# Kernel optimization log

Hardware: AMD Instinct MI355X
Metric: run time of the kernel (lower is better)

Reference implementation:

```python
import jax, jax.numpy as jnp
import numpy as np
import math

B, S, HID = 2, 2048, 2048
NH, NKV, HD = 16, 4, 128
ROPE_BASE = 10000.0

def _rope(x, position_ids):
    # x: [B, H, S, HD], position_ids: [B, S]
    half = HD // 2
    inv_freq = 1.0 / (ROPE_BASE ** (jnp.arange(0, half, dtype=jnp.float32) / half))
    freqs = position_ids.astype(jnp.float32)[:, :, None] * inv_freq[None, None, :]  # [B,S,half]
    cos = jnp.cos(freqs)[:, None, :, :]  # [B,1,S,half]
    sin = jnp.sin(freqs)[:, None, :, :]
    x1, x2 = x[..., :half], x[..., half:]
    return jnp.concatenate([x1 * cos - x2 * sin, x2 * cos + x1 * sin], axis=-1)

def setup_inputs() -> dict:
    key = jax.random.key(0)
    k1, k2, k3 = jax.random.split(key, 3)
    x = jax.random.normal(k1, (B, S, HID), dtype=jnp.float32)
    position_ids = jnp.broadcast_to(jnp.arange(S, dtype=jnp.int64 if jax.config.jax_enable_x64 else jnp.int32)[None, :], (B, S))
    causal = jnp.tril(jnp.ones((S, S), dtype=bool))
    mask = jnp.where(causal, 0.0, -1e9).astype(jnp.float32)[None, None, :, :]
    w_qkv = jax.random.normal(k2, (NH * HD + 2 * NKV * HD, HID), dtype=jnp.float32) * 0.02
    w_o = jax.random.normal(k3, (HID, HID), dtype=jnp.float32) * 0.02
    return {"x": x, "position_ids": position_ids, "mask": mask, "w_qkv": w_qkv, "w_o": w_o}

def reference(x, position_ids, mask, w_qkv, w_o):
    qkv = x @ w_qkv.T  # [B,S,3072]
    q_dim, kv_dim = NH * HD, NKV * HD
    q = qkv[..., :q_dim].reshape(B, S, NH, HD).transpose(0, 2, 1, 3)          # [B,NH,S,HD]
    k = qkv[..., q_dim:q_dim + kv_dim].reshape(B, S, NKV, HD).transpose(0, 2, 1, 3)
    v = qkv[..., q_dim + kv_dim:].reshape(B, S, NKV, HD).transpose(0, 2, 1, 3)
    q = _rope(q, position_ids)
    k = _rope(k, position_ids)
    n_rep = NH // NKV
    k = jnp.repeat(k, n_rep, axis=1)  # [B,NH,S,HD]
    v = jnp.repeat(v, n_rep, axis=1)
    scores = jnp.einsum('bhqd,bhkd->bhqk', q, k) / math.sqrt(HD) + mask
    attn = jax.nn.softmax(scores, axis=-1)  # dropout p=0.0 -> identity
    out = jnp.einsum('bhqk,bhkd->bhqd', attn, v)
    out = out.transpose(0, 2, 1, 3).reshape(B, S, HID)
    return out @ w_o.T
```

## Files before the change

kernel.cpp:

```cpp
#include <hip/hip_runtime.h>
#include <hip/hip_bf16.h>
#include <cstdint>
#include <cstddef>

typedef unsigned short u16;
typedef __attribute__((ext_vector_type(8))) __bf16 bf16x8;
typedef __attribute__((ext_vector_type(4))) float floatx4;

#define B_    2
#define S_    2048
#define HID_  2048
#define NH_   16
#define NKV_  4
#define HD_   128
#define QKVN_ 3072

__device__ __forceinline__ float bf2f(u16 u) {
  union { unsigned int i; float f; } v; v.i = ((unsigned int)u) << 16; return v.f;
}
__device__ __forceinline__ u16 f2bf(float f) {
  union { float f; unsigned int i; } v; v.f = f;
  unsigned int u = v.i;
  return (u16)((u + 0x7fffu + ((u >> 16) & 1u)) >> 16);
}

#define GLOAD_LDS16(gp, lp)                                                  \
  __builtin_amdgcn_global_load_lds(                                          \
      (__attribute__((address_space(1))) void*)(gp),                         \
      (__attribute__((address_space(3))) void*)(lp), 16, 0, 0)

__global__ __launch_bounds__(256)
void cast_f32_bf16(const float* __restrict__ in, u16* __restrict__ out, int n)
{
  const int i = (blockIdx.x * 256 + threadIdx.x) * 8;
  if (i >= n) return;
  const float4 a = *(const float4*)(in + i);
  const float4 b = *(const float4*)(in + i + 4);
  union { u16 h[8]; uint4 v; } o;
  o.h[0] = f2bf(a.x); o.h[1] = f2bf(a.y); o.h[2] = f2bf(a.z); o.h[3] = f2bf(a.w);
  o.h[4] = f2bf(b.x); o.h[5] = f2bf(b.y); o.h[6] = f2bf(b.z); o.h[7] = f2bf(b.w);
  *(uint4*)(out + i) = o.v;
}

template <bool F32OUT>
__global__ __launch_bounds__(256, 3)
void gemm_bt_128(const u16* __restrict__ A, const u16* __restrict__ W,
                 void* __restrict__ Cv, int N, int K, int lda, int ldc)
{
  __shared__ __align__(16) u16 lA[128 * 64];
  __shared__ __align__(16) u16 lB[128 * 64];
  const int tid  = threadIdx.x;
  const int w    = tid >> 6, ln = tid & 63;
  const int quad = ln >> 4,  l15 = ln & 15;
  const int m0 = blockIdx.y * 128, n0 = blockIdx.x * 128;
  const int waveM = (w >> 1) * 64, waveN = (w & 1) * 64;

  const floatx4 vzero = {0.f, 0.f, 0.f, 0.f};
  floatx4 acc[4][4];
#pragma unroll
  for (int i = 0; i < 4; ++i)
#pragma unroll
    for (int j = 0; j < 4; ++j) acc[i][j] = vzero;

  for (int k0 = 0; k0 < K; k0 += 64) {
    __syncthreads();
#pragma unroll
    for (int p = 0; p < 4; ++p) {
      const int L = (p * 4 + w) * 64 + ln;
      const int row = L >> 3, c = L & 7;
      GLOAD_LDS16(A + (size_t)(m0 + row) * lda + k0 + c * 8, lA + L * 8);
      GLOAD_LDS16(W + (size_t)(n0 + row) * K   + k0 + c * 8, lB + L * 8);
    }
    __syncthreads();
#pragma unroll
    for (int kk = 0; kk < 64; kk += 32) {
      bf16x8 aF[4], bF[4];
      const int cbase = (kk >> 3) + quad;
#pragma unroll
      for (int t = 0; t < 4; ++t) {
        const int rowA = waveM + t * 16 + l15;
        aF[t] = *(const bf16x8*)(lA + rowA * 64 + cbase * 8);
        const int rowB = waveN + t * 16 + l15;
        bF[t] = *(const bf16x8*)(lB + rowB * 64 + cbase * 8);
      }
#pragma unroll
      for (int i = 0; i < 4; ++i)
#pragma unroll
        for (int j = 0; j < 4; ++j)
          acc[i][j] = __builtin_amdgcn_mfma_f32_16x16x32_bf16(aF[i], bF[j], acc[i][j], 0, 0, 0);
    }
  }
#pragma unroll
  for (int i = 0; i < 4; ++i)
#pragma unroll
    for (int r = 0; r < 4; ++r) {
      const int row = m0 + waveM + i * 16 + quad * 4 + r;
      if (F32OUT) {
        float* cp = (float*)Cv + (size_t)row * ldc + n0 + waveN + l15;
#pragma unroll
        for (int j = 0; j < 4; ++j) cp[j * 16] = acc[i][j][r];
      } else {
        u16* cp = (u16*)Cv + (size_t)row * ldc + n0 + waveN + l15;
#pragma unroll
        for (int j = 0; j < 4; ++j) cp[j * 16] = f2bf(acc[i][j][r]);
      }
    }
}

__global__ __launch_bounds__(256)
void rope_inplace(u16* __restrict__ qkv)
{
  const int s = blockIdx.x, b = blockIdx.y;
  const int tid = threadIdx.x;
  __shared__ float cs[64], sn[64];
  if (tid < 64) {
    const float inv = powf(10000.0f, -((float)tid) / 64.0f);
    float s_, c_;
    sincosf((float)s * inv, &s_, &c_);
    cs[tid] = c_; sn[tid] = s_;
  }
  __syncthreads();
  u16* base = qkv + ((size_t)b * S_ + s) * QKVN_;
  for (int p = tid; p < NH_ * 64; p += 256) {
    const int h = p >> 6, i = p & 63;
    u16* hp = base + h * 128;
    const float x1 = bf2f(hp[i]);
    const float x2 = bf2f(hp[64 + i]);
    hp[i]      = f2bf(x1 * cs[i] - x2 * sn[i]);
    hp[64 + i] = f2bf(x2 * cs[i] + x1 * sn[i]);
  }
  for (int p = tid; p < NKV_ * 64; p += 256) {
    const int h = p >> 6, i = p & 63;
    u16* hp = base + NH_ * HD_ + h * 128;
    const float x1 = bf2f(hp[i]);
    const float x2 = bf2f(hp[64 + i]);
    hp[i]      = f2bf(x1 * cs[i] - x2 * sn[i]);
    hp[64 + i] = f2bf(x2 * cs[i] + x1 * sn[i]);
  }
}

__global__ __launch_bounds__(256)
void v_transpose(const u16* __restrict__ qkv, u16* __restrict__ vt)
{
  const int s0  = blockIdx.x * 64;
  const int kvh = blockIdx.y;
  const int b   = blockIdx.z;
  const int tid = threadIdx.x;
  __shared__ u16 lT[128 * 73];

  const u16* vsrc = qkv + ((size_t)b * S_ + s0) * QKVN_
                    + NH_ * HD_ + NKV_ * HD_ + kvh * HD_;
#pragma unroll
  for (int p = 0; p < 4; ++p) {
    const int idx = p * 256 + tid;
    const int r = idx >> 4, c = idx & 15;
    union { uint4 v; u16 h[8]; } u;
    u.v = *(const uint4*)(vsrc + (size_t)r * QKVN_ + c * 8);
#pragma unroll
    for (int j = 0; j < 8; ++j)
      lT[(c * 8 + j) * 73 + r] = u.h[j];
  }
  __syncthreads();
  u16* vdst = vt + ((size_t)(b * NKV_ + kvh) * HD_) * S_ + s0;
#pragma unroll
  for (int p = 0; p < 4; ++p) {
    const int idx = p * 256 + tid;
    const int d = idx >> 3, rc = idx & 7;
    union { uint4 v; u16 h[8]; } o;
#pragma unroll
    for (int j = 0; j < 8; ++j)
      o.h[j] = lT[d * 73 + rc * 8 + j];
    *(uint4*)(vdst + (size_t)d * S_ + rc * 8) = o.v;
  }
}

#define LPP 68
#define KSLOT(key, s) ((key) * 128 + (((s) ^ ((key) & 7)) * 8))
#define VSLOT(d, s)   ((d) * 64  + (((s) ^ ((d) & 7)) * 8))

__global__ __launch_bounds__(256, 2)
void flash_attn(u16* __restrict__ qkv, const u16* __restrict__ vt_ws)
{
  const int pi = blockIdx.x;
  const int h  = blockIdx.y;
  const int b  = blockIdx.z;
  const int tid  = threadIdx.x;
  const int w    = tid >> 6, ln = tid & 63;
  const int quad = ln >> 4,  l15 = ln & 15;
  const int kvh  = h >> 2;

  const int qtA = 31 - pi, qtB = pi;
  const int itA = qtA + 1;
  const int nIt = itA + qtB + 1;

  __shared__ __align__(16) u16 lK[2][64 * 128];
  __shared__ __align__(16) u16 lVt[2][128 * 64];
  __shared__ __align__(16) u16 lP[4][16 * LPP];

  const float scale = 0.08838834764831845f;
  const u16* kbase = qkv + (size_t)b * S_ * QKVN_ + NH_ * HD_ + kvh * HD_;
  const u16* vbase = vt_ws + (size_t)(b * NKV_ + kvh) * HD_ * S_;
  const floatx4 vzero = {0.f, 0.f, 0.f, 0.f};

  bf16x8 qFA[4], qFB[4];
  {
    const u16* qpA = qkv + ((size_t)(b * S_) + qtA * 64 + w * 16 + l15) * QKVN_ + h * HD_;
    const u16* qpB = qkv + ((size_t)(b * S_) + qtB * 64 + w * 16 + l15) * QKVN_ + h * HD_;
#pragma unroll
    for (int c = 0; c < 4; ++c) {
      qFA[c] = *(const bf16x8*)(qpA + c * 32 + quad * 8);
      qFB[c] = *(const bf16x8*)(qpB + c * 32 + quad * 8);
    }
  }

  float m_i[4], l_i[4];
  floatx4 Oacc[8];
#pragma unroll
  for (int r = 0; r < 4; ++r) { m_i[r] = -1e30f; l_i[r] = 0.f; }
#pragma unroll
  for (int t = 0; t < 8; ++t) Oacc[t] = vzero;

  bf16x8 qF[4];
#pragma unroll
  for (int c = 0; c < 4; ++c) qF[c] = qFA[c];
  int qtC = qtA;
  int qrow0 = qtA * 64 + w * 16;

#pragma unroll
  for (int p = 0; p < 4; ++p) {
    const int idx = (w * 4 + p) * 64 + ln;
    const int key = idx >> 4, ks = idx & 15;
    GLOAD_LDS16(kbase + (size_t)key * QKVN_ + ((ks ^ (key & 7)) * 8),
                lK[0] + (w * 4 + p) * 512);
    const int d = idx >> 3, vs = idx & 7;
    GLOAD_LDS16(vbase + (size_t)d * S_ + ((vs ^ (d & 7)) * 8),
                lVt[0] + (w * 4 + p) * 512);
  }

#pragma unroll 1
  for (int it = 0; it < nIt; ++it) {
    const int ktC = (it < itA) ? it : (it - itA);
    const u16* lKc = lK[it & 1];
    const u16* lVc = lVt[it & 1];
    const bool pf = (it + 1 < nIt);
    if (pf) {
      const int ktN = (it + 1 < itA) ? (it + 1) : (it + 1 - itA);
      u16* lKn = lK[(it + 1) & 1];
      u16* lVn = lVt[(it + 1) & 1];
#pragma unroll
      for (int p = 0; p < 4; ++p) {
        const int idx = (w * 4 + p) * 64 + ln;
        const int key = idx >> 4, ks = idx & 15;
        GLOAD_LDS16(kbase + (size_t)(ktN * 64 + key) * QKVN_ + ((ks ^ (key & 7)) * 8),
                    lKn + (w * 4 + p) * 512);
        const int d = idx >> 3, vs = idx & 7;
        GLOAD_LDS16(vbase + (size_t)d * S_ + ktN * 64 + ((vs ^ (d & 7)) * 8),
                    lVn + (w * 4 + p) * 512);
      }
      asm volatile("s_waitcnt vmcnt(8)" ::: "memory");
    } else {
      asm volatile("s_waitcnt vmcnt(0)" ::: "memory");
    }
    __builtin_amdgcn_s_barrier();
    __builtin_amdgcn_sched_barrier(0);

    floatx4 sc[4];
    __builtin_amdgcn_s_setprio(1);
#pragma unroll
    for (int nt = 0; nt < 4; ++nt) {
      floatx4 a = vzero;
      const int keyloc = nt * 16 + l15;
#pragma unroll
      for (int c = 0; c < 4; ++c) {
        const bf16x8 kF = *(const bf16x8*)(lKc + KSLOT(keyloc, c * 4 + quad));
        a = __builtin_amdgcn_mfma_f32_16x16x32_bf16(qF[c], kF, a, 0, 0, 0);
      }
      sc[nt] = a;
    }
    __builtin_amdgcn_s_setprio(0);

    float pr[4][4];
#pragma unroll
    for (int r = 0; r < 4; ++r) {
      const int qrow = qrow0 + quad * 4 + r;
      float s[4];
#pragma unroll
      for (int nt = 0; nt < 4; ++nt) {
        const int key0 = ktC * 64 + nt * 16 + l15;
        s[nt] = sc[nt][r] * scale + ((key0 <= qrow) ? 0.f : -1e9f);
      }
      float mx = fmaxf(fmaxf(s[0], s[1]), fmaxf(s[2], s[3]));
#pragma unroll
      for (int off = 1; off < 16; off <<= 1) mx = fmaxf(mx, __shfl_xor(mx, off, 64));
      const float mn = fmaxf(m_i[r], mx);
      const float alpha = __expf(m_i[r] - mn);
      float sm = 0.f;
#pragma unroll
      for (int nt = 0; nt < 4; ++nt) {
        const float p = __expf(s[nt] - mn);
        pr[nt][r] = p;
        sm += p;
      }
#pragma unroll
      for (int off = 1; off < 16; off <<= 1) sm += __shfl_xor(sm, off, 64);
      l_i[r] = l_i[r] * alpha + sm;
      m_i[r] = mn;
#pragma unroll
      for (int t = 0; t < 8; ++t) Oacc[t][r] *= alpha;
    }

#pragma unroll
    for (int nt = 0; nt < 4; ++nt)
#pragma unroll
      for (int r = 0; r < 4; ++r)
        lP[w][(quad * 4 + r) * LPP + nt * 16 + l15] = f2bf(pr[nt][r]);

    {
      const bf16x8 pF0 = *(const bf16x8*)(&lP[w][l15 * LPP + quad * 8]);
      const bf16x8 pF1 = *(const bf16x8*)(&lP[w][l15 * LPP + 32 + quad * 8]);
      __builtin_amdgcn_s_setprio(1);
#pragma unroll
      for (int t = 0; t < 8; ++t) {
        const int d = t * 16 + l15;
        const bf16x8 vF0 = *(const bf16x8*)(lVc + VSLOT(d, quad));
        const bf16x8 vF1 = *(const bf16x8*)(lVc + VSLOT(d, 4 + quad));
        Oacc[t] = __builtin_amdgcn_mfma_f32_16x16x32_bf16(pF0, vF0, Oacc[t], 0, 0, 0);
        Oacc[t] = __builtin_amdgcn_mfma_f32_16x16x32_bf16(pF1, vF1, Oacc[t], 0, 0, 0);
      }
      __builtin_amdgcn_s_setprio(0);
    }

    if (ktC == qtC) {
      float linv[4];
#pragma unroll
      for (int r = 0; r < 4; ++r) linv[r] = 1.0f / l_i[r];
#pragma unroll
      for (int t = 0; t < 8; ++t) {
        const int d = t * 16 + l15;
#pragma unroll
        for (int r = 0; r < 4; ++r) {
          const int qrow = qrow0 + quad * 4 + r;
          qkv[((size_t)(b * S_ + qrow)) * QKVN_ + h * HD_ + d] =
              f2bf(Oacc[t][r] * linv[r]);
        }
      }
      if (pf) {
        qtC = qtB;
        qrow0 = qtB * 64 + w * 16;
#pragma unroll
        for (int c = 0; c < 4; ++c) qF[c] = qFB[c];
#pragma unroll
        for (int r = 0; r < 4; ++r) { m_i[r] = -1e30f; l_i[r] = 0.f; }
#pragma unroll
        for (int t = 0; t < 8; ++t) Oacc[t] = vzero;
      }
    }

    __builtin_amdgcn_s_barrier();
  }
}

extern "C" void kernel_launch(void* const* d_in, const int* in_sizes, int n_in,
                              void* d_out, int out_size, void* d_ws, size_t ws_size,
                              hipStream_t stream)
{
  (void)in_sizes; (void)n_in; (void)out_size; (void)ws_size;
  const float* x     = (const float*)d_in[0];
  const float* w_qkv = (const float*)d_in[3];
  const float* w_o   = (const float*)d_in[4];
  float* out = (float*)d_out;

  const int nX  = B_ * S_ * HID_;
  const int nWq = QKVN_ * HID_;
  const int nWo = HID_ * HID_;

  u16* ws    = (u16*)d_ws;
  u16* qkv   = ws;
  u16* slotW = qkv + (size_t)(B_ * S_) * QKVN_;
  u16* xb    = (u16*)d_out;
  u16* vt_ws = (u16*)d_out;

  const dim3 blk(256);
  cast_f32_bf16<<<nX  / 2048, blk, 0, stream>>>(x,     xb,    nX);
  cast_f32_bf16<<<nWq / 2048, blk, 0, stream>>>(w_qkv, slotW, nWq);
  gemm_bt_128<false><<<dim3(QKVN_ / 128, (B_ * S_) / 128), blk, 0, stream>>>(
      xb, slotW, qkv, QKVN_, HID_, HID_, QKVN_);
  rope_inplace<<<dim3(S_, B_), blk, 0, stream>>>(qkv);
  v_transpose<<<dim3(S_ / 64, NKV_, B_), blk, 0, stream>>>(qkv, vt_ws);
  cast_f32_bf16<<<nWo / 2048, blk, 0, stream>>>(w_o, slotW, nWo);
  flash_attn<<<dim3(16, NH_, B_), blk, 0, stream>>>(qkv, vt_ws);
  gemm_bt_128<true><<<dim3(HID_ / 128, (B_ * S_) / 128), blk, 0, stream>>>(
      qkv, slotW, out, HID_, HID_, QKVN_, HID_);
}
```

Before: 341.2 us.

## Add 256x256-tile 512-thread GEMM for QKV projection with double-buffered LDS

Adds a new GEMM kernel with 256x256 output tiles, 8 waves, and double-buffered global-to-LDS loads in 128KB of dynamic shared memory, and uses it for the QKV projection. Larger tiles raise arithmetic intensity and cut global traffic per FLOP. The grid shrinks to 12x16=192 blocks, which may underfill a 256-CU device, and 128KB of LDS per block limits occupancy. The old 128-tile kernel's launch bounds also change from 3 to 2 blocks per CU.

Result: no change. 340.2 us (-0.3%).

```diff
diff --git a/kernel.cpp b/kernel.cpp
--- a/kernel.cpp
+++ b/kernel.cpp
@@ -43,7 +43,115 @@
 }
 
 template <bool F32OUT>
-__global__ __launch_bounds__(256, 3)
+__global__ __launch_bounds__(512, 2)
+void gemm_bt_256(const u16* __restrict__ A, const u16* __restrict__ W,
+                 void* __restrict__ Cv, int K, int lda, int ldc)
+{
+  extern __shared__ __align__(16) u16 smem[];
+  u16* lA = smem;
+  u16* lB = smem + 32768;
+
+  const int tid  = threadIdx.x;
+  const int wid  = tid >> 6, ln = tid & 63;
+  const int quad = ln >> 4,  l15 = ln & 15;
+  const int wr = wid >> 2, wc = wid & 3;
+  const int m0 = blockIdx.y * 256, n0 = blockIdx.x * 256;
+
+  const floatx4 vzero = {0.f, 0.f, 0.f, 0.f};
+  floatx4 acc[8][4];
+#pragma unroll
+  for (int i = 0; i < 8; ++i)
+#pragma unroll
+    for (int j = 0; j < 4; ++j) acc[i][j] = vzero;
+
+  const int NT = K >> 6;
+
+#define STAGE256(kt, buf)                                                     \
+  {                                                                           \
+    _Pragma("unroll")                                                         \
+    for (int p = 0; p < 4; ++p) {                                             \
+      const int L = (wid * 4 + p) * 64 + ln;                                  \
+      const int row = L >> 3, c = L & 7;                                      \
+      const int cs = (c ^ (row & 7)) * 8;                                     \
+      GLOAD_LDS16(A + (size_t)(m0 + row) * lda + (kt) * 64 + cs,              \
+                  lA + (buf) * 16384 + L * 8);                                \
+      GLOAD_LDS16(W + (size_t)(n0 + row) * K + (kt) * 64 + cs,                \
+                  lB + (buf) * 16384 + L * 8);                                \
+    }                                                                         \
+  }
+
+  STAGE256(0, 0);
+
+#pragma unroll 1
+  for (int t = 0; t < NT; ++t) {
+    if (t + 1 < NT) {
+      STAGE256(t + 1, (t + 1) & 1);
+      asm volatile("s_waitcnt vmcnt(8)" ::: "memory");
+    } else {
+      asm volatile("s_waitcnt vmcnt(0)" ::: "memory");
+    }
+    __builtin_amdgcn_s_barrier();
+    __builtin_amdgcn_sched_barrier(0);
+
+    const u16* a = lA + (t & 1) * 16384;
+    const u16* b = lB + (t & 1) * 16384;
+
+    bf16x8 bF[4][2];
+#pragma unroll
+    for (int j = 0; j < 4; ++j)
+#pragma unroll
+      for (int c = 0; c < 2; ++c) {
+        const int row = wc * 64 + j * 16 + l15;
+        const int g = (c * 4 + quad) ^ (row & 7);
+        bF[j][c] = *(const bf16x8*)(b + row * 64 + g * 8);
+      }
+
+#pragma unroll
+    for (int mh = 0; mh < 2; ++mh) {
+      bf16x8 aF[4][2];
+#pragma unroll
+      for (int i = 0; i < 4; ++i)
+#pragma unroll
+        for (int c = 0; c < 2; ++c) {
+          const int row = wr * 128 + mh * 64 + i * 16 + l15;
+          const int g = (c * 4 + quad) ^ (row & 7);
+          aF[i][c] = *(const bf16x8*)(a + row * 64 + g * 8);
+        }
+      __builtin_amdgcn_s_setprio(1);
+#pragma unroll
+      for (int i = 0; i < 4; ++i)
+#pragma unroll
+        for (int j = 0; j < 4; ++j)
+#pragma unroll
+          for (int c = 0; c < 2; ++c)
+            acc[mh * 4 + i][j] = __builtin_amdgcn_mfma_f32_16x16x32_bf16(
+                aF[i][c], bF[j][c], acc[mh * 4 + i][j], 0, 0, 0);
+      __builtin_amdgcn_s_setprio(0);
+    }
+
+    __builtin_amdgcn_s_barrier();
+  }
+#undef STAGE256
+
+#pragma unroll
+  for (int i = 0; i < 8; ++i)
+#pragma unroll
+    for (int r = 0; r < 4; ++r) {
+      const int row = m0 + wr * 128 + i * 16 + quad * 4 + r;
+      if (F32OUT) {
+        float* cp = (float*)Cv + (size_t)row * ldc + n0 + wc * 64 + l15;
+#pragma unroll
+        for (int j = 0; j < 4; ++j) cp[j * 16] = acc[i][j][r];
+      } else {
+        u16* cp = (u16*)Cv + (size_t)row * ldc + n0 + wc * 64 + l15;
+#pragma unroll
+        for (int j = 0; j < 4; ++j) cp[j * 16] = f2bf(acc[i][j][r]);
+      }
+    }
+}
+
+template <bool F32OUT>
+__global__ __launch_bounds__(256, 2)
 void gemm_bt_128(const u16* __restrict__ A, const u16* __restrict__ W,
                  void* __restrict__ Cv, int N, int K, int lda, int ldc)
 {
@@ -383,8 +491,8 @@
   const dim3 blk(256);
   cast_f32_bf16<<<nX  / 2048, blk, 0, stream>>>(x,     xb,    nX);
   cast_f32_bf16<<<nWq / 2048, blk, 0, stream>>>(w_qkv, slotW, nWq);
-  gemm_bt_128<false><<<dim3(QKVN_ / 128, (B_ * S_) / 128), blk, 0, stream>>>(
-      xb, slotW, qkv, QKVN_, HID_, HID_, QKVN_);
+  gemm_bt_256<false><<<dim3(QKVN_ / 256, (B_ * S_) / 256), dim3(512), 131072, stream>>>(
+      xb, slotW, qkv, HID_, HID_, QKVN_);
   rope_inplace<<<dim3(S_, B_), blk, 0, stream>>>(qkv);
   v_transpose<<<dim3(S_ / 64, NKV_, B_), blk, 0, stream>>>(qkv, vt_ws);
   cast_f32_bf16<<<nWo / 2048, blk, 0, stream>>>(w_o, slotW, nWo);
```

## Replace 128x128 GEMM with double-buffered 256x256 eight-wave swizzled kernel

Applied to the files above, without the earlier changes.

Both projection GEMMs move from a 128x128, 4-wave, single-buffered kernel to a 256x256, 8-wave kernel. The new kernel uses 128KB of dynamic LDS with two buffers and XOR-swizzled layout to avoid bank conflicts, interleaves global-to-LDS staging of the next K tile with MFMA quarters, and raises wave priority around the math. The aim is more data reuse per loaded byte and better overlap of loads with compute. In exchange the grids shrink to 192 and 128 blocks, fewer than the CU count, so parts of the device may sit idle. The large LDS footprint also allows only one block per CU.

Result: no change. 343.7 us (+0.7%).

```diff
diff --git a/kernel.cpp b/kernel.cpp
--- a/kernel.cpp
+++ b/kernel.cpp
@@ -42,65 +42,133 @@
   *(uint4*)(out + i) = o.v;
 }
 
+#define STG_A(T, h)                                                          \
+  { _Pragma("unroll") for (int p = 0; p < 2; ++p) {                          \
+      const int L = p * 512 + tid; const int row = L >> 3, c = L & 7;        \
+      GLOAD_LDS16(A + (size_t)(m0 + (h) * 128 + row) * lda + (T) * 64        \
+                    + ((c ^ (row & 7)) * 8),                                 \
+                  lA + ((T) & 1) * 16384 + (h) * 8192 + L * 8); } }
+#define STG_B(T, h)                                                          \
+  { _Pragma("unroll") for (int p = 0; p < 2; ++p) {                          \
+      const int L = p * 512 + tid; const int row = L >> 3, c = L & 7;        \
+      GLOAD_LDS16(W + (size_t)(n0 + (h) * 128 + row) * K + (T) * 64          \
+                    + ((c ^ (row & 7)) * 8),                                 \
+                  lB + ((T) & 1) * 16384 + (h) * 8192 + L * 8); } }
+#define RD_A(mf, kc, buf) (*(const bf16x8*)(lA + (buf) * 16384 + wr * 8192   \
+    + ((mf) * 16 + l15) * 64 + (((kc) * 4 + quad) ^ (l15 & 7)) * 8))
+#define RD_B(nf, kc, buf) (*(const bf16x8*)(lB + (buf) * 16384               \
+    + (wc >> 1) * 8192 + ((wc & 1) * 64 + (nf) * 16 + l15) * 64              \
+    + (((kc) * 4 + quad) ^ (l15 & 7)) * 8))
+#define RDS_A03(buf) { _Pragma("unroll") for (int ii = 0; ii < 4; ++ii) {    \
+    aR[ii][0] = RD_A(ii, 0, buf); aR[ii][1] = RD_A(ii, 1, buf); } }
+#define RDS_A47(buf) { _Pragma("unroll") for (int ii = 0; ii < 4; ++ii) {    \
+    aR[ii][0] = RD_A(ii + 4, 0, buf); aR[ii][1] = RD_A(ii + 4, 1, buf); } }
+#define RDS_B01(buf) { bR[0][0] = RD_B(0, 0, buf); bR[0][1] = RD_B(0, 1, buf); \
+    bR[1][0] = RD_B(1, 0, buf); bR[1][1] = RD_B(1, 1, buf); }
+#define RDS_B23(buf) { bR[2][0] = RD_B(2, 0, buf); bR[2][1] = RD_B(2, 1, buf); \
+    bR[3][0] = RD_B(3, 0, buf); bR[3][1] = RD_B(3, 1, buf); }
+#define MFMAQ(iB, jB)                                                        \
+  { _Pragma("unroll") for (int ii = 0; ii < 4; ++ii)                         \
+    _Pragma("unroll") for (int jj = 0; jj < 2; ++jj)                         \
+    _Pragma("unroll") for (int kc = 0; kc < 2; ++kc)                         \
+      acc[(iB) + ii][(jB) + jj] = __builtin_amdgcn_mfma_f32_16x16x32_bf16(   \
+          aR[ii][kc], bR[(jB) + jj][kc], acc[(iB) + ii][(jB) + jj], 0, 0, 0); }
+#define MID_BAR do { __builtin_amdgcn_s_barrier();                           \
+    asm volatile("s_waitcnt lgkmcnt(0)" ::: "memory");                       \
+    __builtin_amdgcn_sched_barrier(0);                                       \
+    __builtin_amdgcn_s_setprio(1); } while (0)
+#define END_BAR do { __builtin_amdgcn_s_setprio(0);                          \
+    __builtin_amdgcn_sched_barrier(0);                                       \
+    __builtin_amdgcn_s_barrier(); } while (0)
+
 template <bool F32OUT>
-__global__ __launch_bounds__(256, 3)
-void gemm_bt_128(const u16* __restrict__ A, const u16* __restrict__ W,
-                 void* __restrict__ Cv, int N, int K, int lda, int ldc)
-{
-  __shared__ __align__(16) u16 lA[128 * 64];
-  __shared__ __align__(16) u16 lB[128 * 64];
+__global__ __launch_bounds__(512, 2)
+void gemm_bt_256(const u16* __restrict__ A, const u16* __restrict__ W,
+                 void* __restrict__ Cv, int K, int lda, int ldc)
+{
+  extern __shared__ __align__(16) u16 smem[];
+  u16* lA = smem;
+  u16* lB = smem + 32768;
+
   const int tid  = threadIdx.x;
-  const int w    = tid >> 6, ln = tid & 63;
+  const int wid  = tid >> 6, ln = tid & 63;
   const int quad = ln >> 4,  l15 = ln & 15;
-  const int m0 = blockIdx.y * 128, n0 = blockIdx.x * 128;
-  const int waveM = (w >> 1) * 64, waveN = (w & 1) * 64;
+  const int wr = wid >> 2, wc = wid & 3;
+  const int m0 = blockIdx.y * 256, n0 = blockIdx.x * 256;
 
   const floatx4 vzero = {0.f, 0.f, 0.f, 0.f};
-  floatx4 acc[4][4];
-#pragma unroll
-  for (int i = 0; i < 4; ++i)
+  floatx4 acc[8][4];
+#pragma unroll
+  for (int i = 0; i < 8; ++i)
 #pragma unroll
     for (int j = 0; j < 4; ++j) acc[i][j] = vzero;
 
-  for (int k0 = 0; k0 < K; k0 += 64) {
-    __syncthreads();
-#pragma unroll
-    for (int p = 0; p < 4; ++p) {
-      const int L = (p * 4 + w) * 64 + ln;
-      const int row = L >> 3, c = L & 7;
-      GLOAD_LDS16(A + (size_t)(m0 + row) * lda + k0 + c * 8, lA + L * 8);
-      GLOAD_LDS16(W + (size_t)(n0 + row) * K   + k0 + c * 8, lB + L * 8);
-    }
-    __syncthreads();
-#pragma unroll
-    for (int kk = 0; kk < 64; kk += 32) {
-      bf16x8 aF[4], bF[4];
-      const int cbase = (kk >> 3) + quad;
-#pragma unroll
-      for (int t = 0; t < 4; ++t) {
-        const int rowA = waveM + t * 16 + l15;
-        aF[t] = *(const bf16x8*)(lA + rowA * 64 + cbase * 8);
-        const int rowB = waveN + t * 16 + l15;
-        bF[t] = *(const bf16x8*)(lB + rowB * 64 + cbase * 8);
-      }
-#pragma unroll
-      for (int i = 0; i < 4; ++i)
-#pragma unroll
-        for (int j = 0; j < 4; ++j)
-          acc[i][j] = __builtin_amdgcn_mfma_f32_16x16x32_bf16(aF[i], bF[j], acc[i][j], 0, 0, 0);
-    }
-  }
-#pragma unroll
-  for (int i = 0; i < 4; ++i)
+  bf16x8 aR[4][2], bR[4][2];
+
+  const int NT = K >> 6;
+  const int NI = NT >> 1;
+
+  STG_A(0, 0); STG_A(0, 1); STG_B(0, 0); STG_B(0, 1); STG_B(1, 0); STG_B(1, 1);
+  asm volatile("s_waitcnt vmcnt(4)" ::: "memory");
+  __builtin_amdgcn_s_barrier();
+
+#pragma unroll 1
+  for (int i = 0; i < NI; ++i) {
+    const int t = 2 * i;
+    const bool more = (i + 1 < NI);
+
+    RDS_A03(0); RDS_B01(0);
+    STG_A(t + 1, 0);
+    MID_BAR; MFMAQ(0, 0); END_BAR;
+
+    RDS_B23(0);
+    STG_A(t + 1, 1);
+    MID_BAR; MFMAQ(0, 2); END_BAR;
+
+    RDS_A47(0);
+    if (more) STG_B(t + 2, 0);
+    MID_BAR; MFMAQ(4, 0); END_BAR;
+
+    if (more) {
+      STG_B(t + 2, 1);
+      asm volatile("s_waitcnt vmcnt(4)" ::: "memory");
+    } else {
+      asm volatile("s_waitcnt vmcnt(0)" ::: "memory");
+    }
+    MID_BAR; MFMAQ(4, 2); END_BAR;
+
+    RDS_A03(1); RDS_B01(1);
+    if (more) STG_A(t + 2, 0);
+    MID_BAR; MFMAQ(0, 0); END_BAR;
+
+    RDS_B23(1);
+    if (more) STG_A(t + 2, 1);
+    MID_BAR; MFMAQ(0, 2); END_BAR;
+
+    RDS_A47(1);
+    if (more) STG_B(t + 3, 0);
+    MID_BAR; MFMAQ(4, 0); END_BAR;
+
+    if (more) {
+      STG_B(t + 3, 1);
+      asm volatile("s_waitcnt vmcnt(4)" ::: "memory");
+    } else {
+      asm volatile("s_waitcnt vmcnt(0)" ::: "memory");
+    }
+    MID_BAR; MFMAQ(4, 2); END_BAR;
+  }
+
+#pragma unroll
+  for (int i = 0; i < 8; ++i)
 #pragma unroll
     for (int r = 0; r < 4; ++r) {
-      const int row = m0 + waveM + i * 16 + quad * 4 + r;
+      const int row = m0 + wr * 128 + i * 16 + quad * 4 + r;
       if (F32OUT) {
-        float* cp = (float*)Cv + (size_t)row * ldc + n0 + waveN + l15;
+        float* cp = (float*)Cv + (size_t)row * ldc + n0 + wc * 64 + l15;
 #pragma unroll
         for (int j = 0; j < 4; ++j) cp[j * 16] = acc[i][j][r];
       } else {
-        u16* cp = (u16*)Cv + (size_t)row * ldc + n0 + waveN + l15;
+        u16* cp = (u16*)Cv + (size_t)row * ldc + n0 + wc * 64 + l15;
 #pragma unroll
         for (int j = 0; j < 4; ++j) cp[j * 16] = f2bf(acc[i][j][r]);
       }
@@ -383,12 +451,12 @@
   const dim3 blk(256);
   cast_f32_bf16<<<nX  / 2048, blk, 0, stream>>>(x,     xb,    nX);
   cast_f32_bf16<<<nWq / 2048, blk, 0, stream>>>(w_qkv, slotW, nWq);
-  gemm_bt_128<false><<<dim3(QKVN_ / 128, (B_ * S_) / 128), blk, 0, stream>>>(
-      xb, slotW, qkv, QKVN_, HID_, HID_, QKVN_);
+  gemm_bt_256<false><<<dim3(QKVN_ / 256, (B_ * S_) / 256), dim3(512), 131072, stream>>>(
+      xb, slotW, qkv, HID_, HID_, QKVN_);
   rope_inplace<<<dim3(S_, B_), blk, 0, stream>>>(qkv);
   v_transpose<<<dim3(S_ / 64, NKV_, B_), blk, 0, stream>>>(qkv, vt_ws);
   cast_f32_bf16<<<nWo / 2048, blk, 0, stream>>>(w_o, slotW, nWo);
   flash_attn<<<dim3(16, NH_, B_), blk, 0, stream>>>(qkv, vt_ws);
-  gemm_bt_128<true><<<dim3(HID_ / 128, (B_ * S_) / 128), blk, 0, stream>>>(
-      qkv, slotW, out, HID_, HID_, QKVN_, HID_);
-}
+  gemm_bt_256<true><<<dim3(HID_ / 256, (B_ * S_) / 256), dim3(512), 131072, stream>>>(
+      qkv, slotW, out, HID_, QKVN_, HID_);
+}
```

## Double-buffer GEMM LDS tiles with XOR swizzle and async prefetch

Applied to the files above, without the earlier changes.

Restructures the bf16 GEMM main loop to double-buffer the LDS tiles. The next K-tile's global-to-LDS loads are issued before computing the current one, with vmcnt waits instead of full __syncthreads. It also XOR-swizzles the LDS column layout to avoid bank conflicts on fragment reads, and raises wave priority around the MFMA block. Doubling LDS use lowers the occupancy hint from 3 to 2 blocks per CU.

Result: no change. 336.7 us (-1.3%).

```diff
diff --git a/kernel.cpp b/kernel.cpp
--- a/kernel.cpp
+++ b/kernel.cpp
@@ -43,12 +43,12 @@
 }
 
 template <bool F32OUT>
-__global__ __launch_bounds__(256, 3)
+__global__ __launch_bounds__(256, 2)
 void gemm_bt_128(const u16* __restrict__ A, const u16* __restrict__ W,
                  void* __restrict__ Cv, int N, int K, int lda, int ldc)
 {
-  __shared__ __align__(16) u16 lA[128 * 64];
-  __shared__ __align__(16) u16 lB[128 * 64];
+  __shared__ __align__(16) u16 lA[2][128 * 64];
+  __shared__ __align__(16) u16 lB[2][128 * 64];
   const int tid  = threadIdx.x;
   const int w    = tid >> 6, ln = tid & 63;
   const int quad = ln >> 4,  l15 = ln & 15;
@@ -62,34 +62,59 @@
 #pragma unroll
     for (int j = 0; j < 4; ++j) acc[i][j] = vzero;
 
-  for (int k0 = 0; k0 < K; k0 += 64) {
-    __syncthreads();
-#pragma unroll
-    for (int p = 0; p < 4; ++p) {
-      const int L = (p * 4 + w) * 64 + ln;
-      const int row = L >> 3, c = L & 7;
-      GLOAD_LDS16(A + (size_t)(m0 + row) * lda + k0 + c * 8, lA + L * 8);
-      GLOAD_LDS16(W + (size_t)(n0 + row) * K   + k0 + c * 8, lB + L * 8);
-    }
-    __syncthreads();
+  const int NT = K >> 6;
+
+#define STAGE128(kt, buf)                                                     \
+  { _Pragma("unroll")                                                         \
+    for (int p = 0; p < 4; ++p) {                                             \
+      const int L = (p * 4 + w) * 64 + ln;                                    \
+      const int row = L >> 3, c = L & 7;                                      \
+      const int cs = (c ^ (row & 7)) * 8;                                     \
+      GLOAD_LDS16(A + (size_t)(m0 + row) * lda + (kt) * 64 + cs,              \
+                  lA[buf] + L * 8);                                           \
+      GLOAD_LDS16(W + (size_t)(n0 + row) * K + (kt) * 64 + cs,                \
+                  lB[buf] + L * 8);                                           \
+    } }
+
+  STAGE128(0, 0);
+
+#pragma unroll 1
+  for (int t = 0; t < NT; ++t) {
+    if (t + 1 < NT) {
+      STAGE128(t + 1, (t + 1) & 1);
+      asm volatile("s_waitcnt vmcnt(8)" ::: "memory");
+    } else {
+      asm volatile("s_waitcnt vmcnt(0)" ::: "memory");
+    }
+    __builtin_amdgcn_s_barrier();
+    __builtin_amdgcn_sched_barrier(0);
+
+    const u16* a = lA[t & 1];
+    const u16* b = lB[t & 1];
 #pragma unroll
     for (int kk = 0; kk < 64; kk += 32) {
       bf16x8 aF[4], bF[4];
       const int cbase = (kk >> 3) + quad;
 #pragma unroll
-      for (int t = 0; t < 4; ++t) {
-        const int rowA = waveM + t * 16 + l15;
-        aF[t] = *(const bf16x8*)(lA + rowA * 64 + cbase * 8);
-        const int rowB = waveN + t * 16 + l15;
-        bF[t] = *(const bf16x8*)(lB + rowB * 64 + cbase * 8);
-      }
+      for (int tt = 0; tt < 4; ++tt) {
+        const int rowA = waveM + tt * 16 + l15;
+        aF[tt] = *(const bf16x8*)(a + rowA * 64 + (cbase ^ (l15 & 7)) * 8);
+        const int rowB = waveN + tt * 16 + l15;
+        bF[tt] = *(const bf16x8*)(b + rowB * 64 + (cbase ^ (l15 & 7)) * 8);
+      }
+      __builtin_amdgcn_s_setprio(1);
 #pragma unroll
       for (int i = 0; i < 4; ++i)
 #pragma unroll
         for (int j = 0; j < 4; ++j)
           acc[i][j] = __builtin_amdgcn_mfma_f32_16x16x32_bf16(aF[i], bF[j], acc[i][j], 0, 0, 0);
-    }
-  }
+      __builtin_amdgcn_s_setprio(0);
+    }
+
+    __builtin_amdgcn_s_barrier();
+  }
+#undef STAGE128
+
 #pragma unroll
   for (int i = 0; i < 4; ++i)
 #pragma unroll
```
